# Optimization experiments

Hardware: AMD Instinct MI355X
Metric: run time of the kernel (lower is better)

## Reference

```python
import jax, jax.numpy as jnp
import numpy as np

N_HEAD = 16
QMIN, QMAX = 0.0, 255.0  # 8-bit asymmetric


def fake_quantize(x, scale, zp):
    # LearnableFakeQuantize (asymmetric, 8-bit) with straight-through round.
    q = x / scale + zp
    q = q + jax.lax.stop_gradient(jnp.round(q) - q)  # STE round
    q = jnp.clip(q, QMIN, QMAX)
    return (q - zp) * scale


def setup_inputs() -> dict:
    key = jax.random.key(0)
    ks = jax.random.split(key, 4)
    B, T, C = 2, 2048, 1024
    return {
        "hidden_states": jax.random.normal(ks[0], (B, T, C), jnp.float32),
        "W_attn": jax.random.normal(ks[1], (C, 3 * C), jnp.float32) * (1.0 / np.sqrt(C)),
        "b_attn": jnp.zeros((3 * C,), jnp.float32),
        "W_proj": jax.random.normal(ks[2], (C, C), jnp.float32) * (1.0 / np.sqrt(C)),
        "b_proj": jnp.zeros((C,), jnp.float32),
        "kv_scale": jnp.full((1,), 0.05, jnp.float32),
        "kv_zp": jnp.full((1,), 128.0, jnp.float32),
    }


def reference(hidden_states, W_attn, b_attn, W_proj, b_proj, kv_scale, kv_zp):
    B, T, C = hidden_states.shape
    H = N_HEAD
    D = C // H
    qkv = hidden_states @ W_attn + b_attn            # [B,T,3C]
    q, k, v = jnp.split(qkv, 3, axis=2)
    # [B,T,C] -> [B,H,T,D]
    q = q.reshape(B, T, H, D).transpose(0, 2, 1, 3)
    k = k.reshape(B, T, H, D).transpose(0, 2, 1, 3)
    v = v.reshape(B, T, H, D).transpose(0, 2, 1, 3)
    k = fake_quantize(k, kv_scale, kv_zp)
    v = fake_quantize(v, kv_scale, kv_zp)
    scores = jnp.einsum("bhqd,bhkd->bhqk", q, k) / jnp.sqrt(jnp.asarray(D, q.dtype))
    causal = jnp.tril(jnp.ones((T, T), bool))        # bias[:T,:T]
    scores = jnp.where(causal, scores, jnp.asarray(-jnp.inf, scores.dtype))
    attn = jax.nn.softmax(scores, axis=-1)
    out = jnp.einsum("bhqk,bhkd->bhqd", attn, v)     # [B,H,T,D]
    out = out.transpose(0, 2, 1, 3).reshape(B, T, C)
    return out @ W_proj + b_proj
```

## Files before the change

### kernel.cpp

```cpp
#include <hip/hip_runtime.h>
#include <math.h>

#define TB 2048
#define CC 1024
#define NH 16
#define HD 64

typedef __bf16 bf16x8 __attribute__((ext_vector_type(8)));
typedef __bf16 bf16x4 __attribute__((ext_vector_type(4)));
typedef float  f32x4  __attribute__((ext_vector_type(4)));

__device__ inline float exp2fast(float x) { return __builtin_amdgcn_exp2f(x); }

__device__ __forceinline__ void gl_lds16(const __bf16* g, __bf16* l) {
    __builtin_amdgcn_global_load_lds(
        (const __attribute__((address_space(1))) void*)g,
        (__attribute__((address_space(3))) void*)l, 16, 0, 0);
}

__global__ __launch_bounds__(256)
void cvt_kernel(const float* __restrict__ src, __bf16* __restrict__ dst) {
    int i = (blockIdx.x * 256 + threadIdx.x) * 4;
    f32x4 v = *(const f32x4*)&src[i];
    bf16x4 o;
    o.x = (__bf16)v.x; o.y = (__bf16)v.y; o.z = (__bf16)v.z; o.w = (__bf16)v.w;
    *(bf16x4*)&dst[i] = o;
}

__global__ __launch_bounds__(256)
void tpose_kernel(const float* __restrict__ src, __bf16* __restrict__ dst,
                  int K, int N) {
    __shared__ __bf16 L[64][68];
    const int tid = threadIdx.x;
    const int n0 = blockIdx.x * 64, k0 = blockIdx.y * 64;
    #pragma unroll
    for (int i = 0; i < 4; i++) {
        int id = tid + i * 256;
        int r = id >> 4, c = (id & 15) * 4;
        f32x4 v = *(const f32x4*)&src[(size_t)(k0 + r) * N + n0 + c];
        bf16x4 o;
        o.x = (__bf16)v.x; o.y = (__bf16)v.y; o.z = (__bf16)v.z; o.w = (__bf16)v.w;
        *(bf16x4*)&L[r][c] = o;
    }
    __syncthreads();
    #pragma unroll
    for (int i = 0; i < 4; i++) {
        int id = tid + i * 256;
        int nr = id >> 4, kc = (id & 15) * 4;
        bf16x4 o;
        o.x = L[kc + 0][nr]; o.y = L[kc + 1][nr];
        o.z = L[kc + 2][nr]; o.w = L[kc + 3][nr];
        *(bf16x4*)&dst[(size_t)(n0 + nr) * K + k0 + kc] = o;
    }
}

template<int BN, int MODE>
__global__ __launch_bounds__(256)
void gemm_bt(const __bf16* __restrict__ A, const __bf16* __restrict__ Bt,
             const float* __restrict__ bias,
             __bf16* __restrict__ o0, __bf16* __restrict__ o1,
             __bf16* __restrict__ o2, float* __restrict__ of,
             int M, int N, int K,
             const float* __restrict__ scp, const float* __restrict__ zpp)
{
    constexpr int NT = BN / 32;
    __shared__ __bf16 Asm[128][32];
    __shared__ __bf16 Bsm[BN][32];

    const int tid  = threadIdx.x;
    const int m0   = blockIdx.y * 128;
    const int n0   = blockIdx.x * BN;
    const int w    = tid >> 6, lane = tid & 63;
    const int wm   = (w & 1) * 64, wn = (w >> 1) * (BN / 2);
    const int r16  = lane & 15, quad = lane >> 4;
    const int srow = lane >> 2;
    const int ssw  = (srow + (srow >> 2)) & 3;
    const int scol = ((lane & 3) ^ ssw) * 8;
    const int rsw  = (r16 + (r16 >> 2)) & 3;
    const int rcol = (quad ^ rsw) * 8;

    f32x4 acc[NT][4];
    #pragma unroll
    for (int i = 0; i < NT; i++)
        #pragma unroll
        for (int j = 0; j < 4; j++) acc[i][j] = 0.f;

    for (int k0 = 0; k0 < K; k0 += 32) {
        #pragma unroll
        for (int p = 0; p < 2; p++)
            gl_lds16(&A[(size_t)(m0 + p * 64 + w * 16 + srow) * K + k0 + scol],
                     &Asm[p * 64 + w * 16][0]);
        #pragma unroll
        for (int p = 0; p < BN / 64; p++)
            gl_lds16(&Bt[(size_t)(n0 + p * 64 + w * 16 + srow) * K + k0 + scol],
                     &Bsm[p * 64 + w * 16][0]);
        __syncthreads();

        bf16x8 af[4], bfr[NT];
        #pragma unroll
        for (int mt = 0; mt < 4; mt++)
            af[mt] = *(const bf16x8*)&Asm[wm + mt * 16 + r16][rcol];
        #pragma unroll
        for (int nt = 0; nt < NT; nt++)
            bfr[nt] = *(const bf16x8*)&Bsm[wn + nt * 16 + r16][rcol];
        #pragma unroll
        for (int nt = 0; nt < NT; nt++)
            #pragma unroll
            for (int mt = 0; mt < 4; mt++)
                acc[nt][mt] = __builtin_amdgcn_mfma_f32_16x16x32_bf16(
                    bfr[nt], af[mt], acc[nt][mt], 0, 0, 0);
        __syncthreads();
    }

    const float sc = scp[0];
    const float zp = zpp[0];

    #pragma unroll
    for (int nt = 0; nt < NT; nt++) {
        #pragma unroll
        for (int mt = 0; mt < 4; mt++) {
            int gm = m0 + wm + mt * 16 + r16;
            int gn = n0 + wn + nt * 16 + quad * 4;
            f32x4 val = acc[nt][mt] + *(const f32x4*)&bias[gn];
            if (MODE == 1) {
                *(f32x4*)&of[(size_t)gm * N + gn] = val;
            } else {
                int part = gn >> 10;
                int idx  = gn & 1023;
                int h = idx >> 6, d = idx & 63;
                int b = gm >> 11, t = gm & 2047;
                size_t off = (((size_t)(b * NH + h)) * TB + t) * HD + d;
                bf16x4 st;
                if (part == 0) {
                    #pragma unroll
                    for (int r = 0; r < 4; r++)
                        st[r] = (__bf16)(val[r] * 0.18033688f);
                    *(bf16x4*)&o0[off] = st;
                } else {
                    #pragma unroll
                    for (int r = 0; r < 4; r++) {
                        float qv = val[r] / sc + zp;
                        qv = rintf(qv);
                        qv = fminf(fmaxf(qv, 0.f), 255.f);
                        st[r] = (__bf16)((qv - zp) * sc);
                    }
                    if (part == 1) *(bf16x4*)&o1[off] = st;
                    else           *(bf16x4*)&o2[off] = st;
                }
            }
        }
    }
}

__global__ __launch_bounds__(256, 4)
void attn_mfma(const __bf16* __restrict__ Q, const __bf16* __restrict__ Kg,
               const __bf16* __restrict__ Vg, __bf16* __restrict__ O)
{
    __shared__ alignas(16) __bf16 Ksm[64][72];
    __shared__ alignas(16) __bf16 Vsm[64][72];

    const int tid  = threadIdx.x;
    const int qt   = 31 - (blockIdx.x >> 5);
    const int bh   = blockIdx.x & 31;
    const int q0   = qt * 64;
    const int w    = tid >> 6, lane = tid & 63;
    const int l15  = lane & 15, quad = lane >> 4;
    const int b    = bh >> 4, h = bh & 15;

    const int krow = tid >> 3;
    const int kseg = (tid & 7) * 8;
    const int vkey = tid & 63;
    const int vc   = tid >> 6;

    const __bf16* Kbh = Kg + (size_t)bh * TB * HD;
    const __bf16* Vbh = Vg + (size_t)bh * TB * HD;

    const __bf16* Qrow = Q + ((size_t)bh * TB + q0 + w * 16 + l15) * HD;
    bf16x8 qf0 = *(const bf16x8*)&Qrow[quad * 8];
    bf16x8 qf1 = *(const bf16x8*)&Qrow[32 + quad * 8];

    const int rbase = (l15 >> 2) * 8 + (l15 & 3);

    bf16x8 af_l;
    {
        __bf16 v = (l15 == 0) ? (__bf16)1.0f : (__bf16)0.0f;
        #pragma unroll
        for (int j = 0; j < 8; j++) af_l[j] = v;
    }

    f32x4 acc_o[4], acc_l;
    #pragma unroll
    for (int nt = 0; nt < 4; nt++) acc_o[nt] = 0.f;
    acc_l = 0.f;
    float mrun = -3.0e38f;

    bf16x8 kpre0 = *(const bf16x8*)&Kbh[(size_t)krow * HD + kseg];
    bf16x8 kpre1 = *(const bf16x8*)&Kbh[(size_t)(32 + krow) * HD + kseg];
    bf16x8 vpre0 = *(const bf16x8*)&Vbh[(size_t)vkey * HD + vc * 8];
    bf16x8 vpre1 = *(const bf16x8*)&Vbh[(size_t)vkey * HD + (4 + vc) * 8];

    for (int kt = 0; kt <= qt; kt++) {
        __syncthreads();
        *(bf16x8*)&Ksm[krow][kseg]      = kpre0;
        *(bf16x8*)&Ksm[32 + krow][kseg] = kpre1;
        #pragma unroll
        for (int j = 0; j < 8; j++) {
            Vsm[vc * 8 + j][vkey]      = vpre0[j];
            Vsm[32 + vc * 8 + j][vkey] = vpre1[j];
        }
        __syncthreads();

        if (kt < qt) {
            const __bf16* Kn = Kbh + (size_t)(kt + 1) * 64 * HD;
            const __bf16* Vn = Vbh + (size_t)(kt + 1) * 64 * HD;
            kpre0 = *(const bf16x8*)&Kn[(size_t)krow * HD + kseg];
            kpre1 = *(const bf16x8*)&Kn[(size_t)(32 + krow) * HD + kseg];
            vpre0 = *(const bf16x8*)&Vn[(size_t)vkey * HD + vc * 8];
            vpre1 = *(const bf16x8*)&Vn[(size_t)vkey * HD + (4 + vc) * 8];
        }

        const bool diag = (kt == qt);

        f32x4 s[4];
        #pragma unroll
        for (int nt = 0; nt < 4; nt++) s[nt] = 0.f;
        #pragma unroll
        for (int nt = 0; nt < 4; nt++) {
            if (diag && (nt & 1) && w < 2) continue;
            int row = rbase + (nt & 1) * 32 + ((nt >> 1) << 2);
            bf16x8 kf0 = *(const bf16x8*)&Ksm[row][quad * 8];
            bf16x8 kf1 = *(const bf16x8*)&Ksm[row][32 + quad * 8];
            s[nt] = __builtin_amdgcn_mfma_f32_16x16x32_bf16(kf0, qf0, s[nt], 0, 0, 0);
            s[nt] = __builtin_amdgcn_mfma_f32_16x16x32_bf16(kf1, qf1, s[nt], 0, 0, 0);
        }

        if (diag) {
            #pragma unroll
            for (int nt = 0; nt < 4; nt++) {
                int koff = (nt & 1) * 32 + ((nt >> 1) << 2) + quad * 8;
                #pragma unroll
                for (int r = 0; r < 4; r++)
                    if (koff + r > w * 16 + l15) s[nt][r] = -3.0e38f;
            }
        }

        float mx = s[0][0];
        #pragma unroll
        for (int nt = 0; nt < 4; nt++)
            #pragma unroll
            for (int r = 0; r < 4; r++) mx = fmaxf(mx, s[nt][r]);
        mx = fmaxf(mx, __shfl_xor(mx, 16));
        mx = fmaxf(mx, __shfl_xor(mx, 32));

        float mnew  = fmaxf(mrun, mx);
        float alpha = exp2fast(mrun - mnew);
        mrun = mnew;
        #pragma unroll
        for (int nt = 0; nt < 4; nt++)
            #pragma unroll
            for (int r = 0; r < 4; r++) acc_o[nt][r] *= alpha;
        acc_l[0] *= alpha;

        float p[4][4];
        #pragma unroll
        for (int nt = 0; nt < 4; nt++)
            #pragma unroll
            for (int r = 0; r < 4; r++) p[nt][r] = exp2fast(s[nt][r] - mnew);

        bf16x8 pf0, pf1;
        #pragma unroll
        for (int j = 0; j < 4; j++) {
            pf0[j]     = (__bf16)p[0][j];
            pf0[4 + j] = (__bf16)p[2][j];
            pf1[j]     = (__bf16)p[1][j];
            pf1[4 + j] = (__bf16)p[3][j];
        }

        acc_l = __builtin_amdgcn_mfma_f32_16x16x32_bf16(af_l, pf0, acc_l, 0, 0, 0);
        acc_l = __builtin_amdgcn_mfma_f32_16x16x32_bf16(af_l, pf1, acc_l, 0, 0, 0);

        #pragma unroll
        for (int nt = 0; nt < 4; nt++) {
            bf16x8 vf0 = *(const bf16x8*)&Vsm[nt * 16 + l15][quad * 8];
            bf16x8 vf1 = *(const bf16x8*)&Vsm[nt * 16 + l15][32 + quad * 8];
            acc_o[nt] = __builtin_amdgcn_mfma_f32_16x16x32_bf16(vf0, pf0, acc_o[nt], 0, 0, 0);
            acc_o[nt] = __builtin_amdgcn_mfma_f32_16x16x32_bf16(vf1, pf1, acc_o[nt], 0, 0, 0);
        }
    }

    float lall = __shfl(acc_l[0], l15);
    float inv  = 1.f / lall;
    size_t trow = (size_t)(b * TB) + q0 + w * 16 + l15;
    #pragma unroll
    for (int nt = 0; nt < 4; nt++) {
        bf16x4 st;
        #pragma unroll
        for (int r = 0; r < 4; r++) st[r] = (__bf16)(acc_o[nt][r] * inv);
        *(bf16x4*)&O[trow * CC + h * HD + nt * 16 + quad * 4] = st;
    }
}

extern "C" void kernel_launch(void* const* d_in, const int* in_sizes, int n_in,
                              void* d_out, int out_size, void* d_ws, size_t ws_size,
                              hipStream_t stream) {
    (void)in_sizes; (void)n_in; (void)out_size; (void)ws_size;
    const float* hidden   = (const float*)d_in[0];
    const float* W_attn   = (const float*)d_in[1];
    const float* b_attn   = (const float*)d_in[2];
    const float* W_proj   = (const float*)d_in[3];
    const float* b_proj   = (const float*)d_in[4];
    const float* kv_scale = (const float*)d_in[5];
    const float* kv_zp    = (const float*)d_in[6];
    float* out = (float*)d_out;

    __bf16* hb  = (__bf16*)d_ws;
    __bf16* wat = hb  + (size_t)4096 * 1024;
    __bf16* wpt = wat + (size_t)3072 * 1024;
    __bf16* qws = wpt + (size_t)1024 * 1024;
    __bf16* kws = qws + (size_t)2 * NH * TB * HD;
    __bf16* vws = kws + (size_t)2 * NH * TB * HD;
    __bf16* ows = vws + (size_t)2 * NH * TB * HD;

    cvt_kernel<<<4096, 256, 0, stream>>>(hidden, hb);
    tpose_kernel<<<dim3(48, 16), 256, 0, stream>>>(W_attn, wat, 1024, 3072);
    tpose_kernel<<<dim3(16, 16), 256, 0, stream>>>(W_proj, wpt, 1024, 1024);

    gemm_bt<128, 0><<<dim3(24, 32), 256, 0, stream>>>(
        hb, wat, b_attn, qws, kws, vws, nullptr, 4096, 3072, 1024, kv_scale, kv_zp);

    attn_mfma<<<dim3(32 * 32), 256, 0, stream>>>(qws, kws, vws, ows);

    gemm_bt<64, 1><<<dim3(16, 32), 256, 0, stream>>>(
        ows, wpt, b_proj, nullptr, nullptr, nullptr, out, 4096, 1024, 1024,
        kv_scale, kv_zp);
}
```

Measured before the change: 194.0 us.

## Merge prep kernels into one launch and double GEMM K-tile to 64

Combines the fp32-to-bf16 conversion and both weight transposes into a single kernel launch, dispatched by block index, to cut launch overhead. Doubles the GEMM K-step from 32 to 64, with a new XOR swizzle for 64-wide LDS rows. Each tile now runs two MFMA sub-steps, which halves the number of barriers and loop iterations. The cost is twice the LDS per block, which may reduce occupancy.

```diff
diff --git a/kernel.cpp b/kernel.cpp
--- a/kernel.cpp
+++ b/kernel.cpp
@@ -19,20 +19,31 @@
 }
 
 __global__ __launch_bounds__(256)
-void cvt_kernel(const float* __restrict__ src, __bf16* __restrict__ dst) {
-    int i = (blockIdx.x * 256 + threadIdx.x) * 4;
-    f32x4 v = *(const f32x4*)&src[i];
-    bf16x4 o;
-    o.x = (__bf16)v.x; o.y = (__bf16)v.y; o.z = (__bf16)v.z; o.w = (__bf16)v.w;
-    *(bf16x4*)&dst[i] = o;
-}
-
-__global__ __launch_bounds__(256)
-void tpose_kernel(const float* __restrict__ src, __bf16* __restrict__ dst,
-                  int K, int N) {
+void prep_kernel(const float* __restrict__ hidden, __bf16* __restrict__ hb,
+                 const float* __restrict__ Wa, __bf16* __restrict__ wat,
+                 const float* __restrict__ Wp, __bf16* __restrict__ wpt)
+{
     __shared__ __bf16 L[64][68];
     const int tid = threadIdx.x;
-    const int n0 = blockIdx.x * 64, k0 = blockIdx.y * 64;
+    const int bid = blockIdx.x;
+    if (bid < 4096) {
+        int i = (bid * 256 + tid) * 4;
+        f32x4 v = *(const f32x4*)&hidden[i];
+        bf16x4 o;
+        o.x = (__bf16)v.x; o.y = (__bf16)v.y; o.z = (__bf16)v.z; o.w = (__bf16)v.w;
+        *(bf16x4*)&hb[i] = o;
+        return;
+    }
+    const float* src; __bf16* dst; int N, n0, k0;
+    if (bid < 4096 + 768) {
+        int t = bid - 4096;
+        src = Wa; dst = wat; N = 3072;
+        n0 = (t % 48) * 64; k0 = (t / 48) * 64;
+    } else {
+        int t = bid - 4864;
+        src = Wp; dst = wpt; N = 1024;
+        n0 = (t % 16) * 64; k0 = (t / 16) * 64;
+    }
     #pragma unroll
     for (int i = 0; i < 4; i++) {
         int id = tid + i * 256;
@@ -50,7 +61,7 @@
         bf16x4 o;
         o.x = L[kc + 0][nr]; o.y = L[kc + 1][nr];
         o.z = L[kc + 2][nr]; o.w = L[kc + 3][nr];
-        *(bf16x4*)&dst[(size_t)(n0 + nr) * K + k0 + kc] = o;
+        *(bf16x4*)&dst[(size_t)(n0 + nr) * 1024 + k0 + kc] = o;
     }
 }
 
@@ -64,8 +75,8 @@
              const float* __restrict__ scp, const float* __restrict__ zpp)
 {
     constexpr int NT = BN / 32;
-    __shared__ __bf16 Asm[128][32];
-    __shared__ __bf16 Bsm[BN][32];
+    __shared__ __bf16 Asm[128][64];
+    __shared__ __bf16 Bsm[BN][64];
 
     const int tid  = threadIdx.x;
     const int m0   = blockIdx.y * 128;
@@ -73,11 +84,9 @@
     const int w    = tid >> 6, lane = tid & 63;
     const int wm   = (w & 1) * 64, wn = (w >> 1) * (BN / 2);
     const int r16  = lane & 15, quad = lane >> 4;
-    const int srow = lane >> 2;
-    const int ssw  = (srow + (srow >> 2)) & 3;
-    const int scol = ((lane & 3) ^ ssw) * 8;
-    const int rsw  = (r16 + (r16 >> 2)) & 3;
-    const int rcol = (quad ^ rsw) * 8;
+    const int srow = lane >> 3;
+    const int scol = ((lane & 7) ^ srow) * 8;
+    const int rsw  = r16 & 7;
 
     f32x4 acc[NT][4];
     #pragma unroll
@@ -85,30 +94,34 @@
         #pragma unroll
         for (int j = 0; j < 4; j++) acc[i][j] = 0.f;
 
-    for (int k0 = 0; k0 < K; k0 += 32) {
-        #pragma unroll
-        for (int p = 0; p < 2; p++)
-            gl_lds16(&A[(size_t)(m0 + p * 64 + w * 16 + srow) * K + k0 + scol],
-                     &Asm[p * 64 + w * 16][0]);
-        #pragma unroll
-        for (int p = 0; p < BN / 64; p++)
-            gl_lds16(&Bt[(size_t)(n0 + p * 64 + w * 16 + srow) * K + k0 + scol],
-                     &Bsm[p * 64 + w * 16][0]);
+    for (int k0 = 0; k0 < K; k0 += 64) {
+        #pragma unroll
+        for (int p = 0; p < 4; p++)
+            gl_lds16(&A[(size_t)(m0 + w * 32 + p * 8 + srow) * K + k0 + scol],
+                     &Asm[w * 32 + p * 8][0]);
+        #pragma unroll
+        for (int p = 0; p < BN / 32; p++)
+            gl_lds16(&Bt[(size_t)(n0 + w * (BN / 4) + p * 8 + srow) * K + k0 + scol],
+                     &Bsm[w * (BN / 4) + p * 8][0]);
         __syncthreads();
 
-        bf16x8 af[4], bfr[NT];
-        #pragma unroll
-        for (int mt = 0; mt < 4; mt++)
-            af[mt] = *(const bf16x8*)&Asm[wm + mt * 16 + r16][rcol];
-        #pragma unroll
-        for (int nt = 0; nt < NT; nt++)
-            bfr[nt] = *(const bf16x8*)&Bsm[wn + nt * 16 + r16][rcol];
-        #pragma unroll
-        for (int nt = 0; nt < NT; nt++)
+        #pragma unroll
+        for (int ks = 0; ks < 2; ks++) {
+            const int col = ((ks * 4 + quad) ^ rsw) * 8;
+            bf16x8 af[4], bfr[NT];
             #pragma unroll
             for (int mt = 0; mt < 4; mt++)
-                acc[nt][mt] = __builtin_amdgcn_mfma_f32_16x16x32_bf16(
-                    bfr[nt], af[mt], acc[nt][mt], 0, 0, 0);
+                af[mt] = *(const bf16x8*)&Asm[wm + mt * 16 + r16][col];
+            #pragma unroll
+            for (int nt = 0; nt < NT; nt++)
+                bfr[nt] = *(const bf16x8*)&Bsm[wn + nt * 16 + r16][col];
+            #pragma unroll
+            for (int nt = 0; nt < NT; nt++)
+                #pragma unroll
+                for (int mt = 0; mt < 4; mt++)
+                    acc[nt][mt] = __builtin_amdgcn_mfma_f32_16x16x32_bf16(
+                        bfr[nt], af[mt], acc[nt][mt], 0, 0, 0);
+        }
         __syncthreads();
     }
 
@@ -321,9 +334,7 @@
     __bf16* vws = kws + (size_t)2 * NH * TB * HD;
     __bf16* ows = vws + (size_t)2 * NH * TB * HD;
 
-    cvt_kernel<<<4096, 256, 0, stream>>>(hidden, hb);
-    tpose_kernel<<<dim3(48, 16), 256, 0, stream>>>(W_attn, wat, 1024, 3072);
-    tpose_kernel<<<dim3(16, 16), 256, 0, stream>>>(W_proj, wpt, 1024, 1024);
+    prep_kernel<<<5120, 256, 0, stream>>>(hidden, hb, W_attn, wat, W_proj, wpt);
 
     gemm_bt<128, 0><<<dim3(24, 32), 256, 0, stream>>>(
         hb, wat, b_attn, qws, kws, vws, nullptr, 4096, 3072, 1024, kv_scale, kv_zp);
```

Result: faster. 182.3 us (-6.0%).
